# Kernel tuning notes

Hardware: AMD Instinct MI355X
Metric: run time of the kernel (lower is better)

## Reference

```python
import jax, jax.numpy as jnp
import numpy as np

H, W = 56, 56
N = H * W
C = 2
THETA_ALPHA = 160.0
THETA_BETA = 3.0
THETA_GAMMA = 3.0
NUM_ITERATIONS = 10


def setup_inputs() -> dict:
    key = jax.random.key(0)
    k1, k2, k3, k4 = jax.random.split(key, 4)
    inputs = jax.random.uniform(k1, (2, H, W), dtype=jnp.float32)
    # Keras 'uniform' initializer: U(-0.05, 0.05)
    sp_w = jax.random.uniform(k2, (C, C), minval=-0.05, maxval=0.05, dtype=jnp.float32)
    bl_w = jax.random.uniform(k3, (C, C), minval=-0.05, maxval=0.05, dtype=jnp.float32)
    compat = jax.random.uniform(k4, (C, C), minval=-0.05, maxval=0.05, dtype=jnp.float32)
    return {"inputs": inputs, "spatial_ker_weights": sp_w,
            "bilateral_ker_weights": bl_w, "compatibility_matrix": compat}


def _sqdist(f):
    # f: [N, D] -> [N, N] squared pairwise distances
    s = jnp.sum(f * f, axis=1)
    return s[:, None] + s[None, :] - 2.0 * (f @ f.T)


def _kernels(rgb_flat):
    # rgb_flat: [N, 3] pixel colors (0..255)
    ys, xs = jnp.meshgrid(jnp.arange(H, dtype=jnp.float32),
                          jnp.arange(W, dtype=jnp.float32), indexing="ij")
    pos = jnp.stack([xs.reshape(-1), ys.reshape(-1)], axis=1)  # [N, 2]
    # spatial (Gaussian) kernel: exp(-||p-q||^2 / (2*gamma^2))
    k_sp = jnp.exp(-0.5 * _sqdist(pos / THETA_GAMMA))
    # bilateral kernel: positions scaled by alpha, colors by beta
    f_bl = jnp.concatenate([pos / THETA_ALPHA, rgb_flat / THETA_BETA], axis=1)
    k_bl = jnp.exp(-0.5 * _sqdist(f_bl))
    return k_sp, k_bl


def reference(inputs, spatial_ker_weights, bilateral_ker_weights, compatibility_matrix):
    unary = inputs[0]            # [H, W], foreground prob
    gray = inputs[1] * 255.0     # [H, W], image intensities scaled as in the layer

    # unaries: [C, H, W] with channel 0 = 1-u, channel 1 = u
    unaries = jnp.stack([1.0 - unary, unary], axis=0).reshape(C, N)

    rgb_flat = jnp.tile(gray.reshape(-1)[:, None], (1, 3))  # [N, 3]

    k_sp, k_bl = _kernels(rgb_flat)
    ones = jnp.ones((N,), dtype=jnp.float32)
    norm_sp = k_sp @ ones  # [N]
    norm_bl = k_bl @ ones  # [N]

    q = unaries
    for i in range(NUM_ITERATIONS):
        softmax_out = q if i == 0 else jax.nn.softmax(q, axis=0)
        spatial_out = (softmax_out @ k_sp) / norm_sp[None, :]     # [C, N]
        bilateral_out = (softmax_out @ k_bl) / norm_bl[None, :]   # [C, N]
        message = spatial_ker_weights @ spatial_out + bilateral_ker_weights @ bilateral_out
        pairwise = compatibility_matrix @ message                 # [C, N]
        q = unaries - pairwise

    cur_q = q.reshape(C, H, W).transpose(1, 2, 0)  # [H, W, C]
    obj_prob = jax.nn.softmax(cur_q, axis=2)[:, :, 1]
    return obj_prob.reshape(1, H, W)
```

## Files before the change

kernel.cpp:

```cpp
#include <hip/hip_runtime.h>


namespace {

constexpr int NPIX = 3136;
constexpr int WIMG = 56;
constexpr int JPB  = 16;
constexpr int NBLK = NPIX / JPB;
constexpr int NTHR = 512;
constexpr int NQ   = NPIX / 4;
constexpr int NBUF = 9;
constexpr int Q2   = NQ - NTHR;
constexpr int NBIN = 128;
constexpr int BANDB = 9;
constexpr int NCHK = 98;
constexpr int CPX  = 32;
constexpr int UTRIP = 16;

constexpr float LOG2E = 1.4426950408889634f;
constexpr float C1 = -LOG2E / 18.0f;
constexpr float C2 = -LOG2E / 51200.0f;
constexpr float C3 = -LOG2E / 6.0f;

constexpr int O_SSH  = 0;
constexpr int O_SSRT = 12544;
constexpr int O_GXY  = 25088;
constexpr int O_MSRT = 50176;
constexpr int O_RANK = 56448;
constexpr int O_OFF  = 62720;
constexpr int O_WSX  = 63248;
constexpr int O_WSY  = 66832;
constexpr int O_LIDX = 70416;
constexpr int POOLSZ = 73552;

#define REDUCE32(v) \
    { v += __shfl_xor(v, 1); v += __shfl_xor(v, 2); v += __shfl_xor(v, 4); \
      v += __shfl_xor(v, 8); v += __shfl_xor(v, 16); }
#define REDUCE64(v) \
    { v += __shfl_xor(v, 1); v += __shfl_xor(v, 2); v += __shfl_xor(v, 4); \
      v += __shfl_xor(v, 8); v += __shfl_xor(v, 16); v += __shfl_xor(v, 32); }

__global__ __launch_bounds__(NTHR) void crf_all(
    const float* __restrict__ inp,
    const float* __restrict__ spw, const float* __restrict__ blw,
    const float* __restrict__ cmw,
    float* sbufs, float* __restrict__ out)
{
    __shared__ __align__(16) unsigned char pool[POOLSZ];
    float*  s_sh  = (float*)(pool + O_SSH);
    float4* s_sh4 = (float4*)(pool + O_SSH);
    float*  s_srt = (float*)(pool + O_SSRT);
    float2* gxy   = (float2*)(pool + O_GXY);
    unsigned short* m_srt = (unsigned short*)(pool + O_MSRT);
    unsigned short* rank  = (unsigned short*)(pool + O_RANK);
    unsigned*       offs  = (unsigned*)(pool + O_OFF);
    float*  wsx   = (float*)(pool + O_WSX);
    float*  wsy   = (float*)(pool + O_WSY);
    unsigned char*  lidx = (unsigned char*)(pool + O_LIDX);
    unsigned short* H  = (unsigned short*)(pool + O_SSH);
    unsigned*       Hz = (unsigned*)(pool + O_SSH);

    const int t   = threadIdx.x;
    const int bid = blockIdx.x;
    const int sub = t & 31;
    const int jl  = t >> 5;
    const int j   = bid * JPB + jl;
    const int xj  = j % WIMG;
    const int yj  = j / WIMG;
    const float xjf = (float)xj, yjf = (float)yj;

    const float uj = inp[j];
    const float gj = inp[NPIX + j] * 255.0f;

    const float e0 = cmw[2] - cmw[0];
    const float e1 = cmw[3] - cmw[1];
    const float alpha = e0 * (spw[0] + blw[0]) + e1 * (spw[2] + blw[2]);
    const float beta  = e0 * (spw[1] - spw[0]) + e1 * (spw[3] - spw[2]);
    const float gamma = e0 * (blw[1] - blw[0]) + e1 * (blw[3] - blw[2]);

    for (int i = t; i < 6272; i += NTHR) Hz[i] = 0u;
    for (int idx = t; idx < JPB * 56; idx += NTHR) {
        const int jlw = idx / 56, p = idx - jlw * 56;
        const int jj = bid * JPB + jlw;
        const float ddx = (float)(jj % WIMG - p);
        const float ddy = (float)(jj / WIMG - p);
        wsx[idx] = __builtin_amdgcn_exp2f(C1 * ddx * ddx);
        wsy[idx] = __builtin_amdgcn_exp2f(C1 * ddy * ddy);
    }
    __syncthreads();
    if (t < NCHK) {
        unsigned short* Hr = H + t * NBIN;
        const int mb = t * CPX;
        for (int i = 0; i < CPX; ++i) {
            int b = (int)(inp[NPIX + mb + i] * 255.0f);
            b = (b > 255 ? 255 : b) >> 1;
            lidx[mb + i] = (unsigned char)Hr[b];
            Hr[b] = (unsigned short)(Hr[b] + 1);
        }
    }
    __syncthreads();
    if (t < NBIN) {
        unsigned run = 0;
        for (int c = 0; c < NCHK; ++c) {
            unsigned short v = H[c * NBIN + t];
            H[c * NBIN + t] = (unsigned short)run;
            run += v;
        }
        offs[t] = run;
    }
    __syncthreads();
    if (t < 64) {
        unsigned v0 = offs[2 * t], v1 = offs[2 * t + 1];
        unsigned sum = v0 + v1;
        unsigned sc = sum;
        for (int d = 1; d < 64; d <<= 1) {
            unsigned n = __shfl_up(sc, d);
            if (t >= d) sc += n;
        }
        unsigned base = sc - sum;
        offs[2 * t] = base;
        offs[2 * t + 1] = base + v0;
        if (t == 63) offs[NBIN] = sc;
    }
    __syncthreads();
    for (int m = t; m < NPIX; m += NTHR) {
        int b = (int)(inp[NPIX + m] * 255.0f);
        b = (b > 255 ? 255 : b) >> 1;
        const int r = (int)offs[b] + (int)H[(m >> 5) * NBIN + b] + (int)lidx[m];
        m_srt[r] = (unsigned short)m;
        rank[m]  = (unsigned short)r;
    }
    __syncthreads();
    for (int p = t; p < NPIX; p += NTHR) {
        const int m = (int)m_srt[p];
        s_srt[p] = inp[m];
        const int yi = (m * 9363) >> 19;
        const int xi = m - yi * 56;
        gxy[p] = make_float2(inp[NPIX + m] * 255.0f, (float)(xi + 64 * yi));
    }
    {
        const float4* u4 = (const float4*)inp;
        for (int q = t; q < NQ; q += NTHR) s_sh4[q] = u4[q];
    }
    __syncthreads();

    float sx, sy;
    {
        float dd = xjf - (float)sub;
        sx = __builtin_amdgcn_exp2f(C1 * dd * dd);
        if (sub + 32 < 56) {
            float d2 = xjf - (float)(sub + 32);
            sx += __builtin_amdgcn_exp2f(C1 * d2 * d2);
        }
        REDUCE32(sx);
        dd = yjf - (float)sub;
        sy = __builtin_amdgcn_exp2f(C1 * dd * dd);
        if (sub + 32 < 56) {
            float d2 = yjf - (float)(sub + 32);
            sy += __builtin_amdgcn_exp2f(C1 * d2 * d2);
        }
        REDUCE32(sy);
    }
    const float rnsp = 1.0f / (sx * sy);

    int bj = (int)gj; bj = (bj > 255 ? 255 : bj) >> 1;
    const int b0 = bj < BANDB ? 0 : bj - BANDB;
    const int b1 = bj + BANDB > NBIN - 1 ? NBIN - 1 : bj + BANDB;
    const int blo = (int)offs[b0];
    const int bhi = (int)offs[b1 + 1];

    auto spatial = [&]() -> float {
        const int wv = t >> 6;
        const int ln = t & 63;
        float v0 = 0.f, v1 = 0.f;
        if (ln < 56) {
            const float4* S = s_sh4 + ln * 14;
            float4 sv[14];
#pragma unroll
            for (int q = 0; q < 14; ++q) sv[q] = S[q];
            const int c0 = wv * 2, c1 = c0 + 1;
            const float4* R0 = (const float4*)(wsx + c0 * 56);
            const float4* R1 = (const float4*)(wsx + c1 * 56);
            float a0 = 0.f, a1 = 0.f;
#pragma unroll
            for (int q = 0; q < 14; ++q) {
                float4 w0 = R0[q], w1 = R1[q];
                a0 = fmaf(w0.x, sv[q].x, a0); a0 = fmaf(w0.y, sv[q].y, a0);
                a0 = fmaf(w0.z, sv[q].z, a0); a0 = fmaf(w0.w, sv[q].w, a0);
                a1 = fmaf(w1.x, sv[q].x, a1); a1 = fmaf(w1.y, sv[q].y, a1);
                a1 = fmaf(w1.z, sv[q].z, a1); a1 = fmaf(w1.w, sv[q].w, a1);
            }
            v0 = wsy[c0 * 56 + ln] * a0;
            v1 = wsy[c1 * 56 + ln] * a1;
        }
        REDUCE64(v0); REDUCE64(v1);
        return (ln < 32) ? v0 : v1;
    };

    auto bilateral = [&](float* nacc_out) -> float {
        float acc = 0.f, nacc = 0.f;
        const int pb = blo + sub;
#pragma unroll
        for (int i = 0; i < UTRIP; ++i) {
            const int pp = pb + i * 32;
            const int pc = pp < bhi ? pp : bhi - 1;
            const float2 gx = gxy[pc];
            const float sv  = s_srt[pc];
            const float yi  = floorf(gx.y * 0.015625f);
            const float xi  = fmaf(-64.f, yi, gx.y);
            const float ux = xi - xjf, vy = yi - yjf;
            const float r2 = fmaf(ux, ux, vy * vy);
            const float dg = gx.x - gj;
            float w = __builtin_amdgcn_exp2f(fmaf(dg * C3, dg, r2 * C2));
            w = (pp < bhi) ? w : 0.0f;
            acc = fmaf(w, sv, acc);
            if (nacc_out) nacc += w;
        }
        for (int pp = pb + UTRIP * 32; pp < bhi; pp += 32) {
            const float2 gx = gxy[pp];
            const float sv  = s_srt[pp];
            const float yi  = floorf(gx.y * 0.015625f);
            const float xi  = fmaf(-64.f, yi, gx.y);
            const float ux = xi - xjf, vy = yi - yjf;
            const float r2 = fmaf(ux, ux, vy * vy);
            const float dg = gx.x - gj;
            const float w = __builtin_amdgcn_exp2f(fmaf(dg * C3, dg, r2 * C2));
            acc = fmaf(w, sv, acc);
            if (nacc_out) nacc += w;
        }
        REDUCE32(acc);
        if (nacc_out) { REDUCE32(nacc); *nacc_out = nacc; }
        return acc;
    };

    auto publish_sync = [&](float s, float* buf) {
        if (sub == 0)
            __hip_atomic_store(&buf[j], s, __ATOMIC_RELAXED,
                               __HIP_MEMORY_SCOPE_AGENT);
        const float4* src = (const float4*)buf;
        float4 a, b;
        const bool two = (t < Q2);
        bool da = false, db = !two;
        for (;;) {
            if (!da)
                asm volatile("global_load_dwordx4 %0, %1, off sc0 sc1"
                             : "=&v"(a) : "v"(src + t));
            if (!db)
                asm volatile("global_load_dwordx4 %0, %1, off sc0 sc1"
                             : "=&v"(b) : "v"(src + NTHR + t));
            asm volatile("s_waitcnt vmcnt(0)" ::: "memory");
            if (!da) da = (fminf(fminf(a.x, a.y), fminf(a.z, a.w)) != 0.0f);
            if (!db) db = (fminf(fminf(b.x, b.y), fminf(b.z, b.w)) != 0.0f);
            if (da && db) break;
        }
        s_sh4[t] = a;
        {
            const int p4 = 4 * t;
            s_srt[rank[p4 + 0]] = a.x;
            s_srt[rank[p4 + 1]] = a.y;
            s_srt[rank[p4 + 2]] = a.z;
            s_srt[rank[p4 + 3]] = a.w;
        }
        if (two) {
            s_sh4[NTHR + t] = b;
            const int p4 = 4 * (NTHR + t);
            s_srt[rank[p4 + 0]] = b.x;
            s_srt[rank[p4 + 1]] = b.y;
            s_srt[rank[p4 + 2]] = b.z;
            s_srt[rank[p4 + 3]] = b.w;
        }
        __syncthreads();
    };

    const float base = 2.0f * uj - 1.0f - alpha;
    float rnbl, s;

    {
        float tsp = spatial();
        float nacc;
        float acc = bilateral(&nacc);
        rnbl = 1.0f / nacc;
        float d = base - beta * (tsp * rnsp) - gamma * (acc * rnbl);
        s = 1.0f / (1.0f + __builtin_amdgcn_exp2f(-d * LOG2E));
    }
    publish_sync(s, sbufs);

    for (int k = 1; k < 10; ++k) {
        float tsp = spatial();
        float acc = bilateral(nullptr);
        float d = base - beta * (tsp * rnsp) - gamma * (acc * rnbl);
        s = 1.0f / (1.0f + __builtin_amdgcn_exp2f(-d * LOG2E));
        if (k < 9) publish_sync(s, sbufs + k * NPIX);
        else if (sub == 0) out[j] = s;
    }
}

}

extern "C" void kernel_launch(void* const* d_in, const int* in_sizes, int n_in,
                              void* d_out, int out_size, void* d_ws, size_t ws_size,
                              hipStream_t stream) {
    const float* inp = (const float*)d_in[0];
    const float* spw = (const float*)d_in[1];
    const float* blw = (const float*)d_in[2];
    const float* cmw = (const float*)d_in[3];
    float* sbufs = (float*)d_ws;
    float* out = (float*)d_out;

    hipMemsetAsync(sbufs, 0, NBUF * NPIX * sizeof(float), stream);
    crf_all<<<dim3(NBLK), dim3(NTHR), 0, stream>>>(inp, spw, blw, cmw,
                                                   sbufs, out);
}
```

Measured before the change: 59.72 us.

## Cache bilateral band weights in LDS across CRF iterations

The first iteration now stores each thread's bilateral kernel weights in a new shared-memory band buffer, so later iterations reuse them instead of recomputing exp2 and the distance terms. Only the fixed unrolled part is cached; any tail beyond it is still recomputed. The unroll depth and band bin width are reduced to keep the cache small. LDS use grows to about 94 KB, which can limit occupancy, and trades transcendental math for extra LDS loads.

```diff
diff --git a/kernel.cpp b/kernel.cpp
--- a/kernel.cpp
+++ b/kernel.cpp
@@ -12,10 +12,10 @@
 constexpr int NBUF = 9;
 constexpr int Q2   = NQ - NTHR;
 constexpr int NBIN = 128;
-constexpr int BANDB = 9;
+constexpr int BANDB = 5;
 constexpr int NCHK = 98;
 constexpr int CPX  = 32;
-constexpr int UTRIP = 16;
+constexpr int UTRIP = 10;
 
 constexpr float LOG2E = 1.4426950408889634f;
 constexpr float C1 = -LOG2E / 18.0f;
@@ -31,7 +31,8 @@
 constexpr int O_WSX  = 63248;
 constexpr int O_WSY  = 66832;
 constexpr int O_LIDX = 70416;
-constexpr int POOLSZ = 73552;
+constexpr int O_WBND = 73552;
+constexpr int POOLSZ = 94032;
 
 #define REDUCE32(v) \
     { v += __shfl_xor(v, 1); v += __shfl_xor(v, 2); v += __shfl_xor(v, 4); \
@@ -57,6 +58,7 @@
     float*  wsx   = (float*)(pool + O_WSX);
     float*  wsy   = (float*)(pool + O_WSY);
     unsigned char*  lidx = (unsigned char*)(pool + O_LIDX);
+    float*  wband = (float*)(pool + O_WBND);
     unsigned short* H  = (unsigned short*)(pool + O_SSH);
     unsigned*       Hz = (unsigned*)(pool + O_SSH);
 
@@ -197,9 +199,10 @@
         return (ln < 32) ? v0 : v1;
     };
 
-    auto bilateral = [&](float* nacc_out) -> float {
+    auto bilateral0 = [&](float* nacc_out) -> float {
         float acc = 0.f, nacc = 0.f;
         const int pb = blo + sub;
+        float* wb = wband + jl * (UTRIP * 32);
 #pragma unroll
         for (int i = 0; i < UTRIP; ++i) {
             const int pp = pb + i * 32;
@@ -213,8 +216,9 @@
             const float dg = gx.x - gj;
             float w = __builtin_amdgcn_exp2f(fmaf(dg * C3, dg, r2 * C2));
             w = (pp < bhi) ? w : 0.0f;
+            wb[i * 32 + sub] = w;
             acc = fmaf(w, sv, acc);
-            if (nacc_out) nacc += w;
+            nacc += w;
         }
         for (int pp = pb + UTRIP * 32; pp < bhi; pp += 32) {
             const float2 gx = gxy[pp];
@@ -226,10 +230,37 @@
             const float dg = gx.x - gj;
             const float w = __builtin_amdgcn_exp2f(fmaf(dg * C3, dg, r2 * C2));
             acc = fmaf(w, sv, acc);
-            if (nacc_out) nacc += w;
+            nacc += w;
+        }
+        REDUCE32(acc); REDUCE32(nacc);
+        *nacc_out = nacc;
+        return acc;
+    };
+
+    auto bilateralK = [&]() -> float {
+        float acc = 0.f;
+        const int pb = blo + sub;
+        const float* wb = wband + jl * (UTRIP * 32);
+#pragma unroll
+        for (int i = 0; i < UTRIP; ++i) {
+            const int pp = pb + i * 32;
+            const int pc = pp < bhi ? pp : bhi - 1;
+            const float w  = wb[i * 32 + sub];
+            const float sv = s_srt[pc];
+            acc = fmaf(w, sv, acc);
+        }
+        for (int pp = pb + UTRIP * 32; pp < bhi; pp += 32) {
+            const float2 gx = gxy[pp];
+            const float sv  = s_srt[pp];
+            const float yi  = floorf(gx.y * 0.015625f);
+            const float xi  = fmaf(-64.f, yi, gx.y);
+            const float ux = xi - xjf, vy = yi - yjf;
+            const float r2 = fmaf(ux, ux, vy * vy);
+            const float dg = gx.x - gj;
+            const float w = __builtin_amdgcn_exp2f(fmaf(dg * C3, dg, r2 * C2));
+            acc = fmaf(w, sv, acc);
         }
         REDUCE32(acc);
-        if (nacc_out) { REDUCE32(nacc); *nacc_out = nacc; }
         return acc;
     };
 
@@ -278,7 +309,7 @@
     {
         float tsp = spatial();
         float nacc;
-        float acc = bilateral(&nacc);
+        float acc = bilateral0(&nacc);
         rnbl = 1.0f / nacc;
         float d = base - beta * (tsp * rnsp) - gamma * (acc * rnbl);
         s = 1.0f / (1.0f + __builtin_amdgcn_exp2f(-d * LOG2E));
@@ -287,7 +318,7 @@
 
     for (int k = 1; k < 10; ++k) {
         float tsp = spatial();
-        float acc = bilateral(nullptr);
+        float acc = bilateralK();
         float d = base - beta * (tsp * rnsp) - gamma * (acc * rnbl);
         s = 1.0f / (1.0f + __builtin_amdgcn_exp2f(-d * LOG2E));
         if (k < 9) publish_sync(s, sbufs + k * NPIX);
```

After: 59.52 us. About the same (-0.3%).
